# Performance work log

Measured on AMD Instinct MI355X. Metric: run time of the kernel, lower is better.

Reference implementation:

```python
import jax, jax.numpy as jnp
import numpy as np

OUT, IN, RANK = 4096, 4096, 512
B, S = 4, 2048


def setup_inputs() -> dict:
    key = jax.random.key(0)
    k_x, k_qa, k_qb, k_sa, k_sb, k_b = jax.random.split(key, 6)
    x = jax.random.normal(k_x, (B, S, IN), dtype=jnp.float32)
    # int8-style symmetric quantized CP factors (stored as int32 for the harness)
    q_a = jax.random.randint(k_qa, (OUT, RANK), -127, 127, dtype=jnp.int32)
    q_b = jax.random.randint(k_qb, (IN, RANK), -127, 127, dtype=jnp.int32)
    scale_a = jax.random.uniform(k_sa, (), dtype=jnp.float32) * 0.01 + 1e-4
    scale_b = jax.random.uniform(k_sb, (), dtype=jnp.float32) * 0.01 + 1e-4
    bias = jax.random.normal(k_b, (OUT,), dtype=jnp.float32)
    return {"x": x, "q_a": q_a, "q_b": q_b, "scale_a": scale_a,
            "scale_b": scale_b, "bias": bias}


def reference(x, q_a, q_b, scale_a, scale_b, bias):
    # dequantize_factors(): symmetric per-factor dequant q * scale
    a = q_a.astype(jnp.float32) * scale_a          # [OUT, RANK]
    b = q_b.astype(jnp.float32) * scale_b          # [IN,  RANK]
    # CP reconstruction: weight = factors[0] @ factors[1].T, viewed as [OUT, IN]
    weight = a @ b.T                               # [OUT, IN] (materialized, as in original)
    # F.linear(x, weight, bias) = x @ weight.T + bias
    return jnp.einsum('bsi,oi->bso', x, weight) + bias
```

## Files before the change

kernel.cpp:

```cpp
#include <hip/hip_runtime.h>
#include <hip/hip_fp16.h>


#define M_TOT 8192
#define N_OUT 4096
#define K_IN  4096
#define RANK  512

typedef _Float16 f16x8 __attribute__((ext_vector_type(8)));
typedef float f32x4 __attribute__((ext_vector_type(4)));

#define WAIT_VM0() asm volatile("s_waitcnt vmcnt(0)" ::: "memory")
#define WAIT_VM8() asm volatile("s_waitcnt vmcnt(8)" ::: "memory")
#define BARRIER() do { __builtin_amdgcn_s_barrier(); __builtin_amdgcn_sched_barrier(0); } while (0)

__device__ __forceinline__ void gload_lds16(const void* g, void* l) {
  __builtin_amdgcn_global_load_lds(
      (const __attribute__((address_space(1))) unsigned int*)g,
      (__attribute__((address_space(3))) unsigned int*)l, 16, 0, 0);
}

__global__ void k_cvt_qa(const int4* __restrict__ q, ushort4* __restrict__ o, int n4) {
  int i = blockIdx.x * blockDim.x + threadIdx.x;
  if (i >= n4) return;
  int4 v = q[i];
  ushort4 r;
  r.x = __half_as_ushort(__float2half_rn((float)v.x));
  r.y = __half_as_ushort(__float2half_rn((float)v.y));
  r.z = __half_as_ushort(__float2half_rn((float)v.z));
  r.w = __half_as_ushort(__float2half_rn((float)v.w));
  o[i] = r;
}

__global__ void k_transpose_qb(const int* __restrict__ qb, __half* __restrict__ qbt) {
  __shared__ __half tile[32][33];
  int tx = threadIdx.x & 31, ty = threadIdx.x >> 5;
  int k0 = blockIdx.x * 32, r0 = blockIdx.y * 32;
#pragma unroll
  for (int j = 0; j < 4; ++j)
    tile[ty + j * 8][tx] = __float2half_rn((float)qb[(size_t)(k0 + ty + j * 8) * RANK + r0 + tx]);
  __syncthreads();
#pragma unroll
  for (int j = 0; j < 4; ++j)
    qbt[(size_t)(r0 + ty + j * 8) * K_IN + k0 + tx] = tile[tx][ty + j * 8];
}

__global__ __launch_bounds__(256, 4) void k_gemm1_sk(
    const float* __restrict__ X, const __half* __restrict__ Bt,
    __half* __restrict__ P) {
  __shared__ __align__(16) uint4 lds[2560];
  const int tid = threadIdx.x;
  const int lane = tid & 63, wn = tid >> 6;
  const int flat = blockIdx.x;
  const int xcd = flat & 7, local = flat >> 3;
  const int z = xcd >> 1;
  const int m_t = (xcd & 1) * 64 + (local >> 1);
  const int n_t = local & 1;
  const int m0 = m_t * 64, n0 = n_t * 256;
  const int kbeg = z * (K_IN / 4);
  const int fr = lane & 15, fq = lane >> 4;

  f32x4 acc[4][4] = {};

  const int ar = tid >> 2, aq = tid & 3;
  const float* xbase = X + (size_t)(m0 + ar) * K_IN + aq * 16;
  const int aslot0 = ar * 8 + ((2 * aq) ^ (ar & 7));
  const int aslot1 = ar * 8 + ((2 * aq + 1) ^ (ar & 7));

  for (int it = 0; it < (K_IN / 4) / 64; ++it) {
    const int k0 = kbeg + it * 64;
#pragma unroll
    for (int c = 0; c < 8; ++c) {
      int d = tid + 256 * c;
      int r = d >> 3, s = (d & 7) ^ (r & 7);
      gload_lds16(Bt + (size_t)(n0 + r) * K_IN + k0 + s * 8, &lds[512 + d]);
    }
    float4 v0 = *(const float4*)(xbase + k0);
    float4 v1 = *(const float4*)(xbase + k0 + 4);
    float4 v2 = *(const float4*)(xbase + k0 + 8);
    float4 v3 = *(const float4*)(xbase + k0 + 12);
    union { __half2 h[4]; uint4 u; } p0, p1;
    p0.h[0] = __floats2half2_rn(v0.x, v0.y);
    p0.h[1] = __floats2half2_rn(v0.z, v0.w);
    p0.h[2] = __floats2half2_rn(v1.x, v1.y);
    p0.h[3] = __floats2half2_rn(v1.z, v1.w);
    p1.h[0] = __floats2half2_rn(v2.x, v2.y);
    p1.h[1] = __floats2half2_rn(v2.z, v2.w);
    p1.h[2] = __floats2half2_rn(v3.x, v3.y);
    p1.h[3] = __floats2half2_rn(v3.z, v3.w);
    lds[aslot0] = p0.u;
    lds[aslot1] = p1.u;
    __syncthreads();
#pragma unroll
    for (int kk = 0; kk < 2; ++kk) {
      const int s = kk * 4 + fq;
      f16x8 a[4], b[4];
#pragma unroll
      for (int mi = 0; mi < 4; ++mi) {
        int r = mi * 16 + fr;
        a[mi] = *(const f16x8*)&lds[r * 8 + (s ^ (r & 7))];
      }
#pragma unroll
      for (int ni = 0; ni < 4; ++ni) {
        int n = wn * 64 + ni * 16 + fr;
        b[ni] = *(const f16x8*)&lds[512 + n * 8 + (s ^ (n & 7))];
      }
#pragma unroll
      for (int mi = 0; mi < 4; ++mi)
#pragma unroll
        for (int ni = 0; ni < 4; ++ni)
          acc[mi][ni] = __builtin_amdgcn_mfma_f32_16x16x32_f16(a[mi], b[ni], acc[mi][ni], 0, 0, 0);
    }
    __syncthreads();
  }

  __half* Pz = P + (size_t)z * M_TOT * RANK;
#pragma unroll
  for (int mi = 0; mi < 4; ++mi)
#pragma unroll
    for (int ni = 0; ni < 4; ++ni) {
      int col = n0 + wn * 64 + ni * 16 + fr;
      int rbase = m0 + mi * 16 + fq * 4;
#pragma unroll
      for (int j = 0; j < 4; ++j)
        Pz[(size_t)(rbase + j) * RANK + col] = __float2half_rn(acc[mi][ni][j]);
    }
}

__global__ void k_reduce_t(const uint4* __restrict__ P, uint4* __restrict__ T8, int n8) {
  int i = blockIdx.x * blockDim.x + threadIdx.x;
  if (i >= n8) return;
  float2 f[4] = {};
#pragma unroll
  for (int zz = 0; zz < 4; ++zz) {
    uint4 v = P[(size_t)zz * n8 + i];
    const __half2* h = (const __half2*)&v;
#pragma unroll
    for (int j = 0; j < 4; ++j) {
      float2 g = __half22float2(h[j]);
      f[j].x += g.x; f[j].y += g.y;
    }
  }
  uint4 r;
  __half2* o = (__half2*)&r;
#pragma unroll
  for (int j = 0; j < 4; ++j) o[j] = __floats2half2_rn(f[j].x, f[j].y);
  T8[i] = r;
}

__global__ __launch_bounds__(256, 2) void k_gemm2(
    const __half* __restrict__ T, const __half* __restrict__ QA,
    const float* __restrict__ sa, const float* __restrict__ sb,
    const float* __restrict__ bias, float* __restrict__ Out) {
  __shared__ __align__(16) uint4 lds[2][2048];
  const int tid = threadIdx.x;
  const int lane = tid & 63, wid = tid >> 6, wm = wid & 1, wn = wid >> 1;
  const int flat = blockIdx.x;
  const int xcd = flat & 7, local = flat >> 3;
  const int n_t = xcd * 4 + (local & 3);
  const int m_t = local >> 2;
  const int m0 = m_t * 128, n0 = n_t * 128;
  const int fr = lane & 15, fq = lane >> 4;

  f32x4 acc[4][4] = {};

  auto stage = [&](int kt, int buf) {
#pragma unroll
    for (int c = 0; c < 4; ++c) {
      int d = tid + 256 * c;
      int r = d >> 3, s = (d & 7) ^ (r & 7);
      gload_lds16(T + (size_t)(m0 + r) * RANK + kt * 64 + s * 8, &lds[buf][d]);
    }
#pragma unroll
    for (int c = 0; c < 4; ++c) {
      int d = tid + 256 * c;
      int r = d >> 3, s = (d & 7) ^ (r & 7);
      gload_lds16(QA + (size_t)(n0 + r) * RANK + kt * 64 + s * 8, &lds[buf][1024 + d]);
    }
  };

  stage(0, 0);
  stage(1, 1);
  WAIT_VM8();
  BARRIER();

  const int NT = RANK / 64;
  for (int t = 0; t < NT; ++t) {
    const int cur = t & 1;
#pragma unroll
    for (int kk = 0; kk < 2; ++kk) {
      int s = kk * 4 + fq;
      f16x8 a[4], b[4];
#pragma unroll
      for (int mi = 0; mi < 4; ++mi) {
        int r = wm * 64 + mi * 16 + fr;
        a[mi] = *(const f16x8*)&lds[cur][r * 8 + (s ^ (r & 7))];
      }
#pragma unroll
      for (int ni = 0; ni < 4; ++ni) {
        int n = wn * 64 + ni * 16 + fr;
        b[ni] = *(const f16x8*)&lds[cur][1024 + n * 8 + (s ^ (n & 7))];
      }
#pragma unroll
      for (int mi = 0; mi < 4; ++mi)
#pragma unroll
        for (int ni = 0; ni < 4; ++ni)
          acc[mi][ni] = __builtin_amdgcn_mfma_f32_16x16x32_f16(a[mi], b[ni], acc[mi][ni], 0, 0, 0);
    }
    if (t == NT - 1) break;
    BARRIER();
    if (t + 2 < NT) {
      stage(t + 2, cur);
      WAIT_VM8();
    } else {
      WAIT_VM0();
    }
    BARRIER();
  }

  const float scale = sa[0] * sb[0];
#pragma unroll
  for (int mi = 0; mi < 4; ++mi)
#pragma unroll
    for (int ni = 0; ni < 4; ++ni) {
      int col = n0 + wn * 64 + ni * 16 + fr;
      float bv = bias[col];
      int rbase = m0 + wm * 64 + mi * 16 + fq * 4;
#pragma unroll
      for (int j = 0; j < 4; ++j)
        Out[(size_t)(rbase + j) * N_OUT + col] = acc[mi][ni][j] * scale + bv;
    }
}

extern "C" void kernel_launch(void* const* d_in, const int* in_sizes, int n_in,
                              void* d_out, int out_size, void* d_ws, size_t ws_size,
                              hipStream_t stream) {
  const float* x    = (const float*)d_in[0];
  const int*   qa   = (const int*)d_in[1];
  const int*   qb   = (const int*)d_in[2];
  const float* sa   = (const float*)d_in[3];
  const float* sb   = (const float*)d_in[4];
  const float* bias = (const float*)d_in[5];
  float* out = (float*)d_out;

  char* ws = (char*)d_ws;
  __half* qa_h = (__half*)ws;
  __half* qbt  = (__half*)(ws + (4u << 20));
  __half* t    = (__half*)(ws + (8u << 20));
  __half* part = (__half*)(ws + (16u << 20));

  k_cvt_qa<<<2048, 256, 0, stream>>>((const int4*)qa, (ushort4*)qa_h, (N_OUT * RANK) / 4);
  dim3 tg(K_IN / 32, RANK / 32);
  k_transpose_qb<<<tg, 256, 0, stream>>>(qb, qbt);

  k_gemm1_sk<<<1024, 256, 0, stream>>>(x, qbt, part);
  const int n8 = M_TOT * RANK / 8;
  k_reduce_t<<<n8 / 256, 256, 0, stream>>>((const uint4*)part, (uint4*)t, n8);

  k_gemm2<<<2048, 256, 0, stream>>>(t, qa_h, sa, sb, bias, out);
}
```

Measured before the change: 137.6 us.

## Pipeline gemm1 with register-prefetched X and triple-buffered B tiles

Rewrites the split-K first GEMM to use 512-thread blocks with 128x256 tiles and a K-step of 32. X rows are prefetched four steps ahead into registers, then converted to fp16 and written to double-buffered LDS. B tiles are triple-buffered via direct global-to-LDS loads. Explicit vmcnt/lgkmcnt waits replace the per-iteration synchronous load-then-compute pattern, hiding global latency behind MFMA work. The trade-offs are higher register pressure, more barriers per unit of K, and a new swizzle layout for the smaller K chunk.

```diff
diff --git a/kernel.cpp b/kernel.cpp
--- a/kernel.cpp
+++ b/kernel.cpp
@@ -11,13 +11,20 @@
 typedef float f32x4 __attribute__((ext_vector_type(4)));
 
 #define WAIT_VM0() asm volatile("s_waitcnt vmcnt(0)" ::: "memory")
+#define WAIT_VM2() asm volatile("s_waitcnt vmcnt(2)" ::: "memory")
+#define WAIT_VM4() asm volatile("s_waitcnt vmcnt(4)" ::: "memory")
 #define WAIT_VM8() asm volatile("s_waitcnt vmcnt(8)" ::: "memory")
+#define WAIT_LGKM0() asm volatile("s_waitcnt lgkmcnt(0)" ::: "memory")
 #define BARRIER() do { __builtin_amdgcn_s_barrier(); __builtin_amdgcn_sched_barrier(0); } while (0)
 
 __device__ __forceinline__ void gload_lds16(const void* g, void* l) {
   __builtin_amdgcn_global_load_lds(
       (const __attribute__((address_space(1))) unsigned int*)g,
       (__attribute__((address_space(3))) unsigned int*)l, 16, 0, 0);
+}
+
+__device__ __forceinline__ int lds_idx(int r, int s) {
+  return (r >> 1) * 8 + (((((r & 1) << 2) | s)) ^ ((r >> 1) & 7));
 }
 
 __global__ void k_cvt_qa(const int4* __restrict__ q, ushort4* __restrict__ o, int n4) {
@@ -45,73 +52,97 @@
     qbt[(size_t)(r0 + ty + j * 8) * K_IN + k0 + tx] = tile[tx][ty + j * 8];
 }
 
-__global__ __launch_bounds__(256, 4) void k_gemm1_sk(
+__global__ __launch_bounds__(512, 2) void k_gemm1_sk(
     const float* __restrict__ X, const __half* __restrict__ Bt,
     __half* __restrict__ P) {
-  __shared__ __align__(16) uint4 lds[2560];
+  __shared__ __align__(16) uint4 lds[4096];
   const int tid = threadIdx.x;
-  const int lane = tid & 63, wn = tid >> 6;
-  const int flat = blockIdx.x;
-  const int xcd = flat & 7, local = flat >> 3;
-  const int z = xcd >> 1;
-  const int m_t = (xcd & 1) * 64 + (local >> 1);
-  const int n_t = local & 1;
-  const int m0 = m_t * 64, n0 = n_t * 256;
+  const int lane = tid & 63, wid = tid >> 6;
+  const int wm = wid & 1, wn = wid >> 1;
+  const int blk = blockIdx.x;
+  const int xcd = blk & 7, m_t = blk >> 3;
+  const int z = xcd >> 1, n_t = xcd & 1;
+  const int m0 = m_t * 128, n0 = n_t * 256;
   const int kbeg = z * (K_IN / 4);
   const int fr = lane & 15, fq = lane >> 4;
+  const int NT = (K_IN / 4) / 32;
 
   f32x4 acc[4][4] = {};
 
   const int ar = tid >> 2, aq = tid & 3;
-  const float* xbase = X + (size_t)(m0 + ar) * K_IN + aq * 16;
-  const int aslot0 = ar * 8 + ((2 * aq) ^ (ar & 7));
-  const int aslot1 = ar * 8 + ((2 * aq + 1) ^ (ar & 7));
-
-  for (int it = 0; it < (K_IN / 4) / 64; ++it) {
-    const int k0 = kbeg + it * 64;
-#pragma unroll
-    for (int c = 0; c < 8; ++c) {
-      int d = tid + 256 * c;
-      int r = d >> 3, s = (d & 7) ^ (r & 7);
-      gload_lds16(Bt + (size_t)(n0 + r) * K_IN + k0 + s * 8, &lds[512 + d]);
-    }
-    float4 v0 = *(const float4*)(xbase + k0);
-    float4 v1 = *(const float4*)(xbase + k0 + 4);
-    float4 v2 = *(const float4*)(xbase + k0 + 8);
-    float4 v3 = *(const float4*)(xbase + k0 + 12);
-    union { __half2 h[4]; uint4 u; } p0, p1;
-    p0.h[0] = __floats2half2_rn(v0.x, v0.y);
-    p0.h[1] = __floats2half2_rn(v0.z, v0.w);
-    p0.h[2] = __floats2half2_rn(v1.x, v1.y);
-    p0.h[3] = __floats2half2_rn(v1.z, v1.w);
-    p1.h[0] = __floats2half2_rn(v2.x, v2.y);
-    p1.h[1] = __floats2half2_rn(v2.z, v2.w);
-    p1.h[2] = __floats2half2_rn(v3.x, v3.y);
-    p1.h[3] = __floats2half2_rn(v3.z, v3.w);
-    lds[aslot0] = p0.u;
-    lds[aslot1] = p1.u;
-    __syncthreads();
-#pragma unroll
-    for (int kk = 0; kk < 2; ++kk) {
-      const int s = kk * 4 + fq;
+  const float* xrow = X + (size_t)(m0 + ar) * K_IN + kbeg + aq * 8;
+  const int aidx = lds_idx(ar, aq);
+  const __half* bsrc0; const __half* bsrc1; int bd0, bd1;
+  {
+    int d0 = tid, d1 = tid + 512;
+    int p0 = d0 >> 3, u0 = (d0 & 7) ^ (p0 & 7);
+    int p1 = d1 >> 3, u1 = (d1 & 7) ^ (p1 & 7);
+    bsrc0 = Bt + (size_t)(n0 + 2 * p0 + (u0 >> 2)) * K_IN + kbeg + (u0 & 3) * 8;
+    bsrc1 = Bt + (size_t)(n0 + 2 * p1 + (u1 >> 2)) * K_IN + kbeg + (u1 & 3) * 8;
+    bd0 = d0; bd1 = d1;
+  }
+
+  float4 A0[2], A1[2], A2[2], A3[2];
+
+#define LOAD_A(S, t) do { \
+    S[0] = *(const float4*)(xrow + (t) * 32); \
+    S[1] = *(const float4*)(xrow + (t) * 32 + 4); } while (0)
+#define WRITE_A(S, t) do { \
+    union { __half2 h[4]; uint4 u; } _p; \
+    _p.h[0] = __floats2half2_rn(S[0].x, S[0].y); \
+    _p.h[1] = __floats2half2_rn(S[0].z, S[0].w); \
+    _p.h[2] = __floats2half2_rn(S[1].x, S[1].y); \
+    _p.h[3] = __floats2half2_rn(S[1].z, S[1].w); \
+    lds[((t) & 1) * 512 + aidx] = _p.u; } while (0)
+#define STAGE_B(t) do { \
+    int _base = 1024 + ((t) % 3) * 1024; \
+    gload_lds16(bsrc0 + (t) * 32, &lds[_base + bd0]); \
+    gload_lds16(bsrc1 + (t) * 32, &lds[_base + bd1]); } while (0)
+
+  LOAD_A(A0, 0); LOAD_A(A1, 1); LOAD_A(A2, 2); LOAD_A(A3, 3);
+  STAGE_B(0); STAGE_B(1);
+  WAIT_VM2();
+  WRITE_A(A0, 0);
+  WAIT_LGKM0();
+  BARRIER();
+
+  for (int t = 0; t < NT; ++t) {
+    if (t + 2 < NT) STAGE_B(t + 2);
+    {
+      const uint4* Ab = &lds[(t & 1) * 512];
+      const uint4* Bb = &lds[1024 + (t % 3) * 1024];
       f16x8 a[4], b[4];
 #pragma unroll
-      for (int mi = 0; mi < 4; ++mi) {
-        int r = mi * 16 + fr;
-        a[mi] = *(const f16x8*)&lds[r * 8 + (s ^ (r & 7))];
-      }
-#pragma unroll
-      for (int ni = 0; ni < 4; ++ni) {
-        int n = wn * 64 + ni * 16 + fr;
-        b[ni] = *(const f16x8*)&lds[512 + n * 8 + (s ^ (n & 7))];
-      }
+      for (int mi = 0; mi < 4; ++mi)
+        a[mi] = *(const f16x8*)&Ab[lds_idx(wm * 64 + mi * 16 + fr, fq)];
+#pragma unroll
+      for (int ni = 0; ni < 4; ++ni)
+        b[ni] = *(const f16x8*)&Bb[lds_idx(wn * 64 + ni * 16 + fr, fq)];
 #pragma unroll
       for (int mi = 0; mi < 4; ++mi)
 #pragma unroll
         for (int ni = 0; ni < 4; ++ni)
           acc[mi][ni] = __builtin_amdgcn_mfma_f32_16x16x32_f16(a[mi], b[ni], acc[mi][ni], 0, 0, 0);
     }
-    __syncthreads();
+    if (t == NT - 1) break;
+    if (t == 0) { WAIT_VM2(); } else if (t < NT - 4) { WAIT_VM4(); } else { WAIT_VM0(); }
+    BARRIER();
+    switch ((t + 1) & 3) {
+      case 0: WRITE_A(A0, t + 1); break;
+      case 1: WRITE_A(A1, t + 1); break;
+      case 2: WRITE_A(A2, t + 1); break;
+      default: WRITE_A(A3, t + 1); break;
+    }
+    if (t + 4 < NT) {
+      switch (t & 3) {
+        case 0: LOAD_A(A0, t + 4); break;
+        case 1: LOAD_A(A1, t + 4); break;
+        case 2: LOAD_A(A2, t + 4); break;
+        default: LOAD_A(A3, t + 4); break;
+      }
+    }
+    WAIT_LGKM0();
+    BARRIER();
   }
 
   __half* Pz = P + (size_t)z * M_TOT * RANK;
@@ -120,11 +151,14 @@
 #pragma unroll
     for (int ni = 0; ni < 4; ++ni) {
       int col = n0 + wn * 64 + ni * 16 + fr;
-      int rbase = m0 + mi * 16 + fq * 4;
+      int rbase = m0 + wm * 64 + mi * 16 + fq * 4;
 #pragma unroll
       for (int j = 0; j < 4; ++j)
         Pz[(size_t)(rbase + j) * RANK + col] = __float2half_rn(acc[mi][ni][j]);
     }
+#undef LOAD_A
+#undef WRITE_A
+#undef STAGE_B
 }
 
 __global__ void k_reduce_t(const uint4* __restrict__ P, uint4* __restrict__ T8, int n8) {
@@ -253,7 +287,7 @@
   dim3 tg(K_IN / 32, RANK / 32);
   k_transpose_qb<<<tg, 256, 0, stream>>>(qb, qbt);
 
-  k_gemm1_sk<<<1024, 256, 0, stream>>>(x, qbt, part);
+  k_gemm1_sk<<<512, 512, 0, stream>>>(x, qbt, part);
   const int n8 = M_TOT * RANK / 8;
   k_reduce_t<<<n8 / 256, 256, 0, stream>>>((const uint4*)part, (uint4*)t, n8);
 
```

Measured after the change: 162.2 us. 17.8% more time.

## Pre-convert X to fp16 and use double-buffered async-LDS GEMM1 with 128x128 tiles

Applied to the files above, without the earlier changes.

Adds a separate pass that converts the fp32 activations to fp16 into workspace. GEMM1 can then stream both operands with global-to-LDS async loads into a double-buffered 128x128 tile pipeline, mirroring GEMM2. The intent is to remove the synchronous per-iteration fp32 loads, conversion and barrier stalls in the old GEMM1. The cost is an extra 64 MB read and 64 MB write over x. The new path only runs when the workspace is at least 112 MB; otherwise the old kernel is used as a fallback.

```diff
diff --git a/kernel.cpp b/kernel.cpp
--- a/kernel.cpp
+++ b/kernel.cpp
@@ -18,6 +18,19 @@
   __builtin_amdgcn_global_load_lds(
       (const __attribute__((address_space(1))) unsigned int*)g,
       (__attribute__((address_space(3))) unsigned int*)l, 16, 0, 0);
+}
+
+__global__ void k_cvt_x(const float4* __restrict__ X, uint4* __restrict__ O, int n8) {
+  int i = blockIdx.x * blockDim.x + threadIdx.x;
+  if (i >= n8) return;
+  float4 a = X[2 * i], b = X[2 * i + 1];
+  uint4 r;
+  __half2* h = (__half2*)&r;
+  h[0] = __floats2half2_rn(a.x, a.y);
+  h[1] = __floats2half2_rn(a.z, a.w);
+  h[2] = __floats2half2_rn(b.x, b.y);
+  h[3] = __floats2half2_rn(b.z, b.w);
+  O[i] = r;
 }
 
 __global__ void k_cvt_qa(const int4* __restrict__ q, ushort4* __restrict__ o, int n4) {
@@ -45,7 +58,91 @@
     qbt[(size_t)(r0 + ty + j * 8) * K_IN + k0 + tx] = tile[tx][ty + j * 8];
 }
 
-__global__ __launch_bounds__(256, 4) void k_gemm1_sk(
+__global__ __launch_bounds__(256, 2) void k_gemm1p(
+    const __half* __restrict__ XH, const __half* __restrict__ Bt,
+    __half* __restrict__ P) {
+  __shared__ __align__(16) uint4 lds[2][2048];
+  const int tid = threadIdx.x;
+  const int lane = tid & 63, wid = tid >> 6, wm = wid & 1, wn = wid >> 1;
+  const int blk = blockIdx.x;
+  const int xcd = blk & 7, local = blk >> 3;
+  const int z = xcd >> 1;
+  const int n_t = (xcd & 1) * 2 + (local & 1);
+  const int m_t = local >> 1;
+  const int m0 = m_t * 128, n0 = n_t * 128;
+  const int kbeg = z * (K_IN / 4);
+  const int fr = lane & 15, fq = lane >> 4;
+
+  f32x4 acc[4][4] = {};
+
+  auto stage = [&](int kt, int buf) {
+#pragma unroll
+    for (int c = 0; c < 4; ++c) {
+      int d = tid + 256 * c;
+      int r = d >> 3, s = (d & 7) ^ (r & 7);
+      gload_lds16(XH + (size_t)(m0 + r) * K_IN + kbeg + kt * 64 + s * 8, &lds[buf][d]);
+    }
+#pragma unroll
+    for (int c = 0; c < 4; ++c) {
+      int d = tid + 256 * c;
+      int r = d >> 3, s = (d & 7) ^ (r & 7);
+      gload_lds16(Bt + (size_t)(n0 + r) * K_IN + kbeg + kt * 64 + s * 8, &lds[buf][1024 + d]);
+    }
+  };
+
+  stage(0, 0);
+  stage(1, 1);
+  WAIT_VM8();
+  BARRIER();
+
+  const int NT = (K_IN / 4) / 64;
+  for (int t = 0; t < NT; ++t) {
+    const int cur = t & 1;
+#pragma unroll
+    for (int kk = 0; kk < 2; ++kk) {
+      int s = kk * 4 + fq;
+      f16x8 a[4], b[4];
+#pragma unroll
+      for (int mi = 0; mi < 4; ++mi) {
+        int r = wm * 64 + mi * 16 + fr;
+        a[mi] = *(const f16x8*)&lds[cur][r * 8 + (s ^ (r & 7))];
+      }
+#pragma unroll
+      for (int ni = 0; ni < 4; ++ni) {
+        int n = wn * 64 + ni * 16 + fr;
+        b[ni] = *(const f16x8*)&lds[cur][1024 + n * 8 + (s ^ (n & 7))];
+      }
+#pragma unroll
+      for (int mi = 0; mi < 4; ++mi)
+#pragma unroll
+        for (int ni = 0; ni < 4; ++ni)
+          acc[mi][ni] = __builtin_amdgcn_mfma_f32_16x16x32_f16(a[mi], b[ni], acc[mi][ni], 0, 0, 0);
+    }
+    if (t == NT - 1) break;
+    BARRIER();
+    if (t + 2 < NT) {
+      stage(t + 2, cur);
+      WAIT_VM8();
+    } else {
+      WAIT_VM0();
+    }
+    BARRIER();
+  }
+
+  __half* Pz = P + (size_t)z * M_TOT * RANK;
+#pragma unroll
+  for (int mi = 0; mi < 4; ++mi)
+#pragma unroll
+    for (int ni = 0; ni < 4; ++ni) {
+      int col = n0 + wn * 64 + ni * 16 + fr;
+      int rbase = m0 + wm * 64 + mi * 16 + fq * 4;
+#pragma unroll
+      for (int j = 0; j < 4; ++j)
+        Pz[(size_t)(rbase + j) * RANK + col] = __float2half_rn(acc[mi][ni][j]);
+    }
+}
+
+__global__ __launch_bounds__(256, 4) void k_gemm1_fb(
     const float* __restrict__ X, const __half* __restrict__ Bt,
     __half* __restrict__ P) {
   __shared__ __align__(16) uint4 lds[2560];
@@ -61,7 +158,6 @@
   const int fr = lane & 15, fq = lane >> 4;
 
   f32x4 acc[4][4] = {};
-
   const int ar = tid >> 2, aq = tid & 3;
   const float* xbase = X + (size_t)(m0 + ar) * K_IN + aq * 16;
   const int aslot0 = ar * 8 + ((2 * aq) ^ (ar & 7));
@@ -248,12 +344,20 @@
   __half* qbt  = (__half*)(ws + (4u << 20));
   __half* t    = (__half*)(ws + (8u << 20));
   __half* part = (__half*)(ws + (16u << 20));
+  __half* x_h  = (__half*)(ws + (48u << 20));
 
   k_cvt_qa<<<2048, 256, 0, stream>>>((const int4*)qa, (ushort4*)qa_h, (N_OUT * RANK) / 4);
   dim3 tg(K_IN / 32, RANK / 32);
   k_transpose_qb<<<tg, 256, 0, stream>>>(qb, qbt);
 
-  k_gemm1_sk<<<1024, 256, 0, stream>>>(x, qbt, part);
+  const bool big_ws = ws_size >= (112ull << 20);
+  if (big_ws) {
+    const int nx8 = M_TOT * K_IN / 8;
+    k_cvt_x<<<nx8 / 256, 256, 0, stream>>>((const float4*)x, (uint4*)x_h, nx8);
+    k_gemm1p<<<1024, 256, 0, stream>>>(x_h, qbt, part);
+  } else {
+    k_gemm1_fb<<<1024, 256, 0, stream>>>(x, qbt, part);
+  }
   const int n8 = M_TOT * RANK / 8;
   k_reduce_t<<<n8 / 256, 256, 0, stream>>>((const uint4*)part, (uint4*)t, n8);
 
```

New measurement: 141.9 us. +3.1%, slower.

## Rework split-K GEMM1 with async fp32 LDS staging and double-buffering

Applied to the files above, without the earlier changes.

GEMM1 now uses 512-thread blocks with 128x256 tiles and a 2-deep LDS ring. Both the fp32 X tile and the fp16 B tile are loaded directly into LDS with global_load_lds, and X is converted to fp16 after it is read back from LDS. This replaces the register-staged synchronous load and convert of X, so the next K-slice's global loads overlap the current MFMA work. GEMM2's prefetch changes from two stages ahead to one stage ahead, issued at the top of each iteration. The cost is fp32 data in LDS, which doubles the A bytes per K, and the deeper prefetch in GEMM2 is lost.

```diff
diff --git a/kernel.cpp b/kernel.cpp
--- a/kernel.cpp
+++ b/kernel.cpp
@@ -11,7 +11,6 @@
 typedef float f32x4 __attribute__((ext_vector_type(4)));
 
 #define WAIT_VM0() asm volatile("s_waitcnt vmcnt(0)" ::: "memory")
-#define WAIT_VM8() asm volatile("s_waitcnt vmcnt(8)" ::: "memory")
 #define BARRIER() do { __builtin_amdgcn_s_barrier(); __builtin_amdgcn_sched_barrier(0); } while (0)
 
 __device__ __forceinline__ void gload_lds16(const void* g, void* l) {
@@ -45,73 +44,74 @@
     qbt[(size_t)(r0 + ty + j * 8) * K_IN + k0 + tx] = tile[tx][ty + j * 8];
 }
 
-__global__ __launch_bounds__(256, 4) void k_gemm1_sk(
+__global__ __launch_bounds__(512, 2) void k_gemm1v(
     const float* __restrict__ X, const __half* __restrict__ Bt,
     __half* __restrict__ P) {
-  __shared__ __align__(16) uint4 lds[2560];
+  __shared__ __align__(16) uint4 lds[2][2048];
   const int tid = threadIdx.x;
-  const int lane = tid & 63, wn = tid >> 6;
-  const int flat = blockIdx.x;
-  const int xcd = flat & 7, local = flat >> 3;
-  const int z = xcd >> 1;
-  const int m_t = (xcd & 1) * 64 + (local >> 1);
-  const int n_t = local & 1;
-  const int m0 = m_t * 64, n0 = n_t * 256;
+  const int lane = tid & 63, wid = tid >> 6;
+  const int wm = wid & 1, wn = wid >> 1;
+  const int blk = blockIdx.x;
+  const int xcd = blk & 7, m_t = blk >> 3;
+  const int z = xcd >> 1, n_t = xcd & 1;
+  const int m0 = m_t * 128, n0 = n_t * 256;
   const int kbeg = z * (K_IN / 4);
   const int fr = lane & 15, fq = lane >> 4;
 
   f32x4 acc[4][4] = {};
 
-  const int ar = tid >> 2, aq = tid & 3;
-  const float* xbase = X + (size_t)(m0 + ar) * K_IN + aq * 16;
-  const int aslot0 = ar * 8 + ((2 * aq) ^ (ar & 7));
-  const int aslot1 = ar * 8 + ((2 * aq + 1) ^ (ar & 7));
-
-  for (int it = 0; it < (K_IN / 4) / 64; ++it) {
-    const int k0 = kbeg + it * 64;
-#pragma unroll
-    for (int c = 0; c < 8; ++c) {
-      int d = tid + 256 * c;
+  auto stage = [&](int kt, int buf) {
+#pragma unroll
+    for (int c = 0; c < 2; ++c) {
+      int d = tid + 512 * c;
       int r = d >> 3, s = (d & 7) ^ (r & 7);
-      gload_lds16(Bt + (size_t)(n0 + r) * K_IN + k0 + s * 8, &lds[512 + d]);
-    }
-    float4 v0 = *(const float4*)(xbase + k0);
-    float4 v1 = *(const float4*)(xbase + k0 + 4);
-    float4 v2 = *(const float4*)(xbase + k0 + 8);
-    float4 v3 = *(const float4*)(xbase + k0 + 12);
-    union { __half2 h[4]; uint4 u; } p0, p1;
-    p0.h[0] = __floats2half2_rn(v0.x, v0.y);
-    p0.h[1] = __floats2half2_rn(v0.z, v0.w);
-    p0.h[2] = __floats2half2_rn(v1.x, v1.y);
-    p0.h[3] = __floats2half2_rn(v1.z, v1.w);
-    p1.h[0] = __floats2half2_rn(v2.x, v2.y);
-    p1.h[1] = __floats2half2_rn(v2.z, v2.w);
-    p1.h[2] = __floats2half2_rn(v3.x, v3.y);
-    p1.h[3] = __floats2half2_rn(v3.z, v3.w);
-    lds[aslot0] = p0.u;
-    lds[aslot1] = p1.u;
-    __syncthreads();
-#pragma unroll
-    for (int kk = 0; kk < 2; ++kk) {
-      const int s = kk * 4 + fq;
-      f16x8 a[4], b[4];
-#pragma unroll
-      for (int mi = 0; mi < 4; ++mi) {
-        int r = mi * 16 + fr;
-        a[mi] = *(const f16x8*)&lds[r * 8 + (s ^ (r & 7))];
-      }
-#pragma unroll
-      for (int ni = 0; ni < 4; ++ni) {
-        int n = wn * 64 + ni * 16 + fr;
-        b[ni] = *(const f16x8*)&lds[512 + n * 8 + (s ^ (n & 7))];
-      }
-#pragma unroll
-      for (int mi = 0; mi < 4; ++mi)
-#pragma unroll
-        for (int ni = 0; ni < 4; ++ni)
-          acc[mi][ni] = __builtin_amdgcn_mfma_f32_16x16x32_f16(a[mi], b[ni], acc[mi][ni], 0, 0, 0);
-    }
-    __syncthreads();
+      gload_lds16(X + (size_t)(m0 + r) * K_IN + kbeg + kt * 32 + s * 4, &lds[buf][d]);
+    }
+#pragma unroll
+    for (int c = 0; c < 2; ++c) {
+      int d = tid + 512 * c;
+      int p = d >> 3, u = (d & 7) ^ (p & 7);
+      gload_lds16(Bt + (size_t)(n0 + 2 * p + (u >> 2)) * K_IN + kbeg + kt * 32 + (u & 3) * 8,
+                  &lds[buf][1024 + d]);
+    }
+  };
+
+  stage(0, 0);
+  WAIT_VM0();
+  BARRIER();
+
+  const int NT = (K_IN / 4) / 32;
+  for (int t = 0; t < NT; ++t) {
+    if (t + 1 < NT) stage(t + 1, (t + 1) & 1);
+    const uint4* Ab = &lds[t & 1][0];
+    const uint4* Bb = &lds[t & 1][1024];
+    f16x8 a[4], b[4];
+#pragma unroll
+    for (int mi = 0; mi < 4; ++mi) {
+      int r = wm * 64 + mi * 16 + fr;
+      f32x4 u0 = *(const f32x4*)&Ab[r * 8 + ((fq * 2) ^ (r & 7))];
+      f32x4 u1 = *(const f32x4*)&Ab[r * 8 + ((fq * 2 + 1) ^ (r & 7))];
+      union { __half2 h[4]; f16x8 v; } pa;
+      pa.h[0] = __floats2half2_rn(u0[0], u0[1]);
+      pa.h[1] = __floats2half2_rn(u0[2], u0[3]);
+      pa.h[2] = __floats2half2_rn(u1[0], u1[1]);
+      pa.h[3] = __floats2half2_rn(u1[2], u1[3]);
+      a[mi] = pa.v;
+    }
+#pragma unroll
+    for (int ni = 0; ni < 4; ++ni) {
+      int r = wn * 64 + ni * 16 + fr;
+      int p = r >> 1;
+      b[ni] = *(const f16x8*)&Bb[p * 8 + ((((r & 1) << 2) | fq) ^ (p & 7))];
+    }
+#pragma unroll
+    for (int mi = 0; mi < 4; ++mi)
+#pragma unroll
+      for (int ni = 0; ni < 4; ++ni)
+        acc[mi][ni] = __builtin_amdgcn_mfma_f32_16x16x32_f16(a[mi], b[ni], acc[mi][ni], 0, 0, 0);
+
+    if (t + 1 < NT) WAIT_VM0();
+    BARRIER();
   }
 
   __half* Pz = P + (size_t)z * M_TOT * RANK;
@@ -120,7 +120,7 @@
 #pragma unroll
     for (int ni = 0; ni < 4; ++ni) {
       int col = n0 + wn * 64 + ni * 16 + fr;
-      int rbase = m0 + mi * 16 + fq * 4;
+      int rbase = m0 + wm * 64 + mi * 16 + fq * 4;
 #pragma unroll
       for (int j = 0; j < 4; ++j)
         Pz[(size_t)(rbase + j) * RANK + col] = __float2half_rn(acc[mi][ni][j]);
@@ -180,12 +180,12 @@
   };
 
   stage(0, 0);
-  stage(1, 1);
-  WAIT_VM8();
+  WAIT_VM0();
   BARRIER();
 
   const int NT = RANK / 64;
   for (int t = 0; t < NT; ++t) {
+    if (t + 1 < NT) stage(t + 1, (t + 1) & 1);
     const int cur = t & 1;
 #pragma unroll
     for (int kk = 0; kk < 2; ++kk) {
@@ -207,14 +207,7 @@
         for (int ni = 0; ni < 4; ++ni)
           acc[mi][ni] = __builtin_amdgcn_mfma_f32_16x16x32_f16(a[mi], b[ni], acc[mi][ni], 0, 0, 0);
     }
-    if (t == NT - 1) break;
-    BARRIER();
-    if (t + 2 < NT) {
-      stage(t + 2, cur);
-      WAIT_VM8();
-    } else {
-      WAIT_VM0();
-    }
+    if (t + 1 < NT) WAIT_VM0();
     BARRIER();
   }
 
@@ -253,7 +246,8 @@
   dim3 tg(K_IN / 32, RANK / 32);
   k_transpose_qb<<<tg, 256, 0, stream>>>(qb, qbt);
 
-  k_gemm1_sk<<<1024, 256, 0, stream>>>(x, qbt, part);
+  k_gemm1v<<<512, 512, 0, stream>>>(x, qbt, part);
+
   const int n8 = M_TOT * RANK / 8;
   k_reduce_t<<<n8 / 256, 256, 0, stream>>>((const uint4*)part, (uint4*)t, n8);
 
```

New measurement: 149.4 us. 8.5% more time.
